# Kernel optimization log

Measured on AMD Instinct MI355X. Metric: run time of the kernel, lower is better.

The kernel has to match this reference:

```python
import jax, jax.numpy as jnp
import numpy as np

N, C, DFF, TMAX = 4, 768, 3072, 20
RMS_EPS = 1e-6
SINK_EPS = 1e-6
POST_MULT = 2.0


def setup_inputs() -> dict:
    key = jax.random.key(0)
    ks = jax.random.split(key, 5)
    B, S = 4, 4096
    x = jax.random.normal(ks[0], (B, S, N, C), dtype=jnp.float32)
    phi = jax.random.normal(ks[1], (N * C, N * N + 2 * N), dtype=jnp.float32) * 0.02
    b = jnp.zeros((N * N + 2 * N,), dtype=jnp.float32)
    alpha_pre = jnp.ones((1,), dtype=jnp.float32)
    alpha_post = jnp.ones((1,), dtype=jnp.float32)
    alpha_res = jnp.ones((1,), dtype=jnp.float32)
    W1 = jax.random.normal(ks[2], (C, DFF), dtype=jnp.float32) * (1.0 / np.sqrt(C))
    b1 = jnp.zeros((DFF,), dtype=jnp.float32)
    W2 = jax.random.normal(ks[3], (DFF, C), dtype=jnp.float32) * (1.0 / np.sqrt(DFF))
    b2 = jnp.zeros((C,), dtype=jnp.float32)
    return {"x": x, "phi": phi, "b": b, "alpha_pre": alpha_pre,
            "alpha_post": alpha_post, "alpha_res": alpha_res,
            "W1": W1, "b1": b1, "W2": W2, "b2": b2}


def _sinkhorn(logits):
    # logits: (..., 16) -> doubly-stochastic (..., 4, 4); rows = logits[..., 4i:4i+4]
    r = logits.reshape(*logits.shape[:-1], N, N)
    r = jnp.exp(r - jnp.max(r, axis=-1, keepdims=True))
    for _ in range(TMAX):
        r = r / (jnp.sum(r, axis=-1, keepdims=True) + SINK_EPS)  # row normalize
        r = r / (jnp.sum(r, axis=-2, keepdims=True) + SINK_EPS)  # column normalize
    return r


def _mhc_forward(x, phi, b, alpha_pre, alpha_post, alpha_res, W1, b1, W2, b2):
    lead = x.shape[:-2]
    x_mat = x.reshape(-1, N * C)
    # fused RMS-norm + linear routing projection
    invr = jax.lax.rsqrt(jnp.mean(x_mat * x_mat, axis=-1, keepdims=True) + RMS_EPS)
    mix = (x_mat @ phi) * invr  # (T, n^2 + 2n)
    h_pre = jax.nn.sigmoid(mix[:, :N] * alpha_pre + b[:N]).reshape(*lead, N)
    h_post = (jax.nn.sigmoid(mix[:, N:2 * N] * alpha_post + b[N:2 * N]) * POST_MULT).reshape(*lead, N)
    h_res = _sinkhorn(mix[:, 2 * N:] * alpha_res + b[2 * N:]).reshape(*lead, N, N)
    # pre-aggregate n streams -> single full-width stream
    x_in = jnp.einsum('...nc,...n->...c', x, h_pre)
    # wrapped sublayer: baseline MLP at full width
    f_out = jax.nn.gelu(x_in @ W1 + b1, approximate=False) @ W2 + b2
    # residual stream mixing + post scatter
    res_gather = jnp.einsum('...ij,...jc->...ic', h_res, x)
    return res_gather + h_post[..., None] * f_out[..., None, :]


def reference(x, phi, b, alpha_pre, alpha_post, alpha_res, W1, b1, W2, b2):
    return _mhc_forward(x, phi, b, alpha_pre, alpha_post, alpha_res, W1, b1, W2, b2)
```

## Files before the change

### kernel.cpp

```cpp
#include <hip/hip_runtime.h>
#include <hip/hip_bf16.h>
#include <stdint.h>

#define NT   16384
#define C_   768
#define DFF_ 3072
#define KX   3072
#define NMIX 24
#define TB   64
#define KSPLIT 4
#define KSEG (KX / KSPLIT)

typedef __attribute__((ext_vector_type(8))) short shortx8;
typedef __attribute__((ext_vector_type(4))) float floatx4;

__device__ __forceinline__ short f2bf(float f) {
  union { float f; uint32_t u; } v; v.f = f;
  uint32_t r = v.u + 0x7fffu + ((v.u >> 16) & 1u);
  return (short)(r >> 16);
}

__device__ __forceinline__ float bf2f(short s) {
  union { uint32_t u; float f; } v;
  v.u = ((uint32_t)(uint16_t)s) << 16;
  return v.f;
}

__device__ __forceinline__ float gelu_f(float v) {
  float u = 1.5957691216057308f * v * (1.0f + 0.044715f * v * v);
  return v / (1.0f + __expf(-u));
}

__global__ void phiT_kernel(const float* __restrict__ phi, float* __restrict__ phiT) {
  int idx = blockIdx.x * 256 + threadIdx.x;
  if (idx < KX * NMIX) {
    int k = idx / NMIX, j = idx - k * NMIX;
    phiT[(size_t)j * KX + k] = phi[idx];
  }
}

__global__ __launch_bounds__(256) void transpose_bf16(const float* __restrict__ in,
                                                      short* __restrict__ out,
                                                      int R, int C) {
  __shared__ float tile[32][33];
  int bx = blockIdx.x * 32;
  int by = blockIdx.y * 32;
  int tx = threadIdx.x & 31, ty = threadIdx.x >> 5;
  #pragma unroll
  for (int i = 0; i < 32; i += 8)
    tile[ty + i][tx] = in[(size_t)(by + ty + i) * C + bx + tx];
  __syncthreads();
  #pragma unroll
  for (int i = 0; i < 32; i += 8)
    out[(size_t)(bx + ty + i) * R + by + tx] = f2bf(tile[tx][ty + i]);
}

__global__ __launch_bounds__(256) void k1a(
    const float* __restrict__ x, const float* __restrict__ phiT,
    float* __restrict__ pmix, float* __restrict__ pssq) {
  __shared__ float xs[TB][132];
  int tid = threadIdx.x;
  int lane = tid & 63;
  int w = tid >> 6;
  int wu = __builtin_amdgcn_readfirstlane(w);
  int t0 = (blockIdx.x >> 2) * TB;
  int slot = blockIdx.x & 3;
  int ks = slot * KSEG;

  float acc[6] = {0.f, 0.f, 0.f, 0.f, 0.f, 0.f};
  float ssq = 0.f;

  for (int kc = ks; kc < ks + KSEG; kc += 128) {
    if (kc != ks) __syncthreads();
    #pragma unroll
    for (int jj = 0; jj < 8; ++jj) {
      int idx = tid + jj * 256;
      int row = idx >> 5, c4 = idx & 31;
      const float4 v = *(const float4*)&x[(size_t)(t0 + row) * KX + kc + c4 * 4];
      *(float4*)&xs[row][c4 * 4] = v;
    }
    __syncthreads();
    #pragma unroll 4
    for (int k4 = 0; k4 < 32; ++k4) {
      const float4 xv = *(const float4*)&xs[lane][k4 * 4];
      if (w == 0) ssq += xv.x * xv.x + xv.y * xv.y + xv.z * xv.z + xv.w * xv.w;
      int kk = kc + k4 * 4;
      #pragma unroll
      for (int jj = 0; jj < 6; ++jj) {
        const float4 p = *(const float4*)&phiT[(size_t)(wu * 6 + jj) * KX + kk];
        acc[jj] += p.x * xv.x + p.y * xv.y + p.z * xv.z + p.w * xv.w;
      }
    }
  }
  if (w == 0) pssq[(size_t)(t0 + lane) * KSPLIT + slot] = ssq;
  #pragma unroll
  for (int jj = 0; jj < 6; ++jj)
    pmix[((size_t)(t0 + lane) * KSPLIT + slot) * NMIX + wu * 6 + jj] = acc[jj];
}

__global__ __launch_bounds__(256) void k1b(
    const float* __restrict__ pmix, const float* __restrict__ pssq,
    const float* __restrict__ bvec, const float* __restrict__ a_pre,
    const float* __restrict__ a_post, const float* __restrict__ a_res,
    float* __restrict__ hpre, float* __restrict__ hpost, float* __restrict__ hres) {
  __shared__ float mixs[TB][NMIX];
  __shared__ float invr_s[TB];
  int tid = threadIdx.x;
  int t0 = blockIdx.x * TB;
  int tq = tid >> 2, r = tid & 3;

  {
    const float* pm = pmix + (size_t)(t0 + tq) * KSPLIT * NMIX;
    float s[6] = {0.f, 0.f, 0.f, 0.f, 0.f, 0.f};
    #pragma unroll
    for (int sl = 0; sl < KSPLIT; ++sl)
      #pragma unroll
      for (int jj = 0; jj < 6; ++jj)
        s[jj] += pm[sl * NMIX + r * 6 + jj];
    #pragma unroll
    for (int jj = 0; jj < 6; ++jj) mixs[tq][r * 6 + jj] = s[jj];
    if (r == 0) {
      const float* ps = pssq + (size_t)(t0 + tq) * KSPLIT;
      float sq = ps[0] + ps[1] + ps[2] + ps[3];
      invr_s[tq] = rsqrtf(sq * (1.0f / KX) + 1e-6f);
    }
  }
  __syncthreads();

  {
    float invr = invr_s[tq];
    float ares = a_res[0];
    float v0 = mixs[tq][8 + r * 4 + 0] * invr * ares + bvec[8 + r * 4 + 0];
    float v1 = mixs[tq][8 + r * 4 + 1] * invr * ares + bvec[8 + r * 4 + 1];
    float v2 = mixs[tq][8 + r * 4 + 2] * invr * ares + bvec[8 + r * 4 + 2];
    float v3 = mixs[tq][8 + r * 4 + 3] * invr * ares + bvec[8 + r * 4 + 3];
    float mx = fmaxf(fmaxf(v0, v1), fmaxf(v2, v3));
    v0 = __expf(v0 - mx); v1 = __expf(v1 - mx); v2 = __expf(v2 - mx); v3 = __expf(v3 - mx);
    for (int it = 0; it < 20; ++it) {
      float s = v0 + v1 + v2 + v3 + 1e-6f;
      float inv = 1.0f / s;
      v0 *= inv; v1 *= inv; v2 *= inv; v3 *= inv;
      float c0 = v0 + __shfl_xor(v0, 1); c0 += __shfl_xor(c0, 2);
      float c1 = v1 + __shfl_xor(v1, 1); c1 += __shfl_xor(c1, 2);
      float c2 = v2 + __shfl_xor(v2, 1); c2 += __shfl_xor(c2, 2);
      float c3 = v3 + __shfl_xor(v3, 1); c3 += __shfl_xor(c3, 2);
      v0 /= (c0 + 1e-6f); v1 /= (c1 + 1e-6f); v2 /= (c2 + 1e-6f); v3 /= (c3 + 1e-6f);
    }
    float* ho = hres + (size_t)(t0 + tq) * 16 + r * 4;
    ho[0] = v0; ho[1] = v1; ho[2] = v2; ho[3] = v3;
    if (r == 0) {
      float apre = a_pre[0];
      float4 hp;
      hp.x = 1.0f / (1.0f + __expf(-(mixs[tq][0] * invr * apre + bvec[0])));
      hp.y = 1.0f / (1.0f + __expf(-(mixs[tq][1] * invr * apre + bvec[1])));
      hp.z = 1.0f / (1.0f + __expf(-(mixs[tq][2] * invr * apre + bvec[2])));
      hp.w = 1.0f / (1.0f + __expf(-(mixs[tq][3] * invr * apre + bvec[3])));
      *(float4*)&hpre[(size_t)(t0 + tq) * 4] = hp;
    } else if (r == 1) {
      float apost = a_post[0];
      float4 hq;
      hq.x = 2.0f / (1.0f + __expf(-(mixs[tq][4] * invr * apost + bvec[4])));
      hq.y = 2.0f / (1.0f + __expf(-(mixs[tq][5] * invr * apost + bvec[5])));
      hq.z = 2.0f / (1.0f + __expf(-(mixs[tq][6] * invr * apost + bvec[6])));
      hq.w = 2.0f / (1.0f + __expf(-(mixs[tq][7] * invr * apost + bvec[7])));
      *(float4*)&hpost[(size_t)(t0 + tq) * 4] = hq;
    }
  }
}

__global__ __launch_bounds__(256) void k1c(
    const float* __restrict__ x, const float* __restrict__ hpre,
    short* __restrict__ x_in) {
  int idx = blockIdx.x * 256 + threadIdx.x;
  int t = idx / 192;
  int c = (idx - t * 192) * 4;
  float4 hp = *(const float4*)&hpre[(size_t)t * 4];
  const float* xr = x + (size_t)t * KX + c;
  float4 x0 = *(const float4*)(xr);
  float4 x1 = *(const float4*)(xr + C_);
  float4 x2 = *(const float4*)(xr + 2 * C_);
  float4 x3 = *(const float4*)(xr + 3 * C_);
  short4 s;
  s.x = f2bf(hp.x * x0.x + hp.y * x1.x + hp.z * x2.x + hp.w * x3.x);
  s.y = f2bf(hp.x * x0.y + hp.y * x1.y + hp.z * x2.y + hp.w * x3.y);
  s.z = f2bf(hp.x * x0.z + hp.y * x1.z + hp.z * x2.z + hp.w * x3.z);
  s.w = f2bf(hp.x * x0.w + hp.y * x1.w + hp.z * x2.w + hp.w * x3.w);
  *(short4*)&x_in[(size_t)t * C_ + c] = s;
}

template <int EPI>
__global__ __launch_bounds__(256, 3) void gemm_bt(
    const short* __restrict__ A, const short* __restrict__ B,
    int M, int N, int K, const float* __restrict__ bias,
    short* __restrict__ outb,
    const float* __restrict__ x, const float* __restrict__ hres,
    const float* __restrict__ hpost, float* __restrict__ out) {
  __shared__ __align__(16) char smem[34816];
  short* As = (short*)smem;
  short* Bs = (short*)(smem + 16384);
  short* cb = (short*)smem;
  int tid = threadIdx.x;
  int lane = tid & 63, w = tid >> 6;
  int nwg = gridDim.x * gridDim.y;
  int lid = blockIdx.y * gridDim.x + blockIdx.x;
  int sid = (lid & 7) * (nwg >> 3) + (lid >> 3);
  int bx = sid % gridDim.x, by = sid / gridDim.x;
  int m0 = by * 128, n0 = bx * 128;
  int wm = (w >> 1) * 64, wn = (w & 1) * 64;
  int lrow = lane & 15, quad = lane >> 4;
  floatx4 acc[4][4] = {};

  int srow = tid >> 2, sslot = tid & 3;
  int srow2 = (tid + 256) >> 2, sslot2 = (tid + 256) & 3;

  auto stage = [&](int buf, int k0) {
    const short* ga = A + (size_t)(m0 + srow) * K + k0 + sslot * 8;
    const short* gb = B + (size_t)(n0 + srow) * K + k0 + sslot * 8;
    __builtin_amdgcn_global_load_lds((const __attribute__((address_space(1))) void*)ga,
        (__attribute__((address_space(3))) void*)&As[buf * 4096 + tid * 8], 16, 0, 0);
    __builtin_amdgcn_global_load_lds((const __attribute__((address_space(1))) void*)gb,
        (__attribute__((address_space(3))) void*)&Bs[buf * 4096 + tid * 8], 16, 0, 0);
    const short* ga2 = A + (size_t)(m0 + srow2) * K + k0 + sslot2 * 8;
    const short* gb2 = B + (size_t)(n0 + srow2) * K + k0 + sslot2 * 8;
    __builtin_amdgcn_global_load_lds((const __attribute__((address_space(1))) void*)ga2,
        (__attribute__((address_space(3))) void*)&As[buf * 4096 + (tid + 256) * 8], 16, 0, 0);
    __builtin_amdgcn_global_load_lds((const __attribute__((address_space(1))) void*)gb2,
        (__attribute__((address_space(3))) void*)&Bs[buf * 4096 + (tid + 256) * 8], 16, 0, 0);
  };

  int ntiles = K >> 5;
  stage(0, 0);
  __syncthreads();
  int cur = 0;
  for (int t = 0; t < ntiles; ++t) {
    if (t + 1 < ntiles) stage(cur ^ 1, (t + 1) << 5);
    shortx8 af[4], bfr[4];
    #pragma unroll
    for (int mi = 0; mi < 4; ++mi)
      af[mi] = *(const shortx8*)&As[cur * 4096 + (wm + mi * 16 + lrow) * 32 + quad * 8];
    #pragma unroll
    for (int ni = 0; ni < 4; ++ni)
      bfr[ni] = *(const shortx8*)&Bs[cur * 4096 + (wn + ni * 16 + lrow) * 32 + quad * 8];
    #pragma unroll
    for (int mi = 0; mi < 4; ++mi)
      #pragma unroll
      for (int ni = 0; ni < 4; ++ni)
        acc[mi][ni] = __builtin_amdgcn_mfma_f32_16x16x32_bf16(af[mi], bfr[ni], acc[mi][ni], 0, 0, 0);
    __syncthreads();
    cur ^= 1;
  }

  float bcol[4];
  #pragma unroll
  for (int ni = 0; ni < 4; ++ni) bcol[ni] = bias[n0 + wn + ni * 16 + lrow];

  #pragma unroll
  for (int mi = 0; mi < 4; ++mi) {
    #pragma unroll
    for (int r = 0; r < 4; ++r) {
      int rr = wm + mi * 16 + quad * 4 + r;
      #pragma unroll
      for (int ni = 0; ni < 4; ++ni) {
        int col = wn + ni * 16 + lrow;
        float v = acc[mi][ni][r] + bcol[ni];
        if (EPI == 1) v = gelu_f(v);
        cb[rr * 136 + col] = f2bf(v);
      }
    }
  }
  __syncthreads();

  int rbase = tid >> 4, ic = tid & 15;
  if (EPI == 1) {
    #pragma unroll
    for (int v = 0; v < 8; ++v) {
      int rr = v * 16 + rbase;
      shortx8 val = *(const shortx8*)&cb[rr * 136 + ic * 8];
      *(shortx8*)&outb[(size_t)(m0 + rr) * N + n0 + ic * 8] = val;
    }
  } else {
    #pragma unroll
    for (int v = 0; v < 8; ++v) {
      int rr = v * 16 + rbase;
      int tr = m0 + rr;
      shortx8 f8 = *(const shortx8*)&cb[rr * 136 + ic * 8];
      float fv[8];
      #pragma unroll
      for (int j = 0; j < 8; ++j) fv[j] = bf2f(f8[j]);
      const float* xr = x + (size_t)tr * KX + n0 + ic * 8;
      float4 xa[4], xb[4];
      #pragma unroll
      for (int n = 0; n < 4; ++n) {
        xa[n] = *(const float4*)(xr + n * 768);
        xb[n] = *(const float4*)(xr + n * 768 + 4);
      }
      const float4* hrp = (const float4*)(hres + (size_t)tr * 16);
      float4 hp4 = *(const float4*)&hpost[(size_t)tr * 4];
      float hpv[4] = {hp4.x, hp4.y, hp4.z, hp4.w};
      float* orow = out + (size_t)tr * KX + n0 + ic * 8;
      #pragma unroll
      for (int n = 0; n < 4; ++n) {
        float4 h = hrp[n];
        float4 oa, ob;
        oa.x = h.x * xa[0].x + h.y * xa[1].x + h.z * xa[2].x + h.w * xa[3].x + hpv[n] * fv[0];
        oa.y = h.x * xa[0].y + h.y * xa[1].y + h.z * xa[2].y + h.w * xa[3].y + hpv[n] * fv[1];
        oa.z = h.x * xa[0].z + h.y * xa[1].z + h.z * xa[2].z + h.w * xa[3].z + hpv[n] * fv[2];
        oa.w = h.x * xa[0].w + h.y * xa[1].w + h.z * xa[2].w + h.w * xa[3].w + hpv[n] * fv[3];
        ob.x = h.x * xb[0].x + h.y * xb[1].x + h.z * xb[2].x + h.w * xb[3].x + hpv[n] * fv[4];
        ob.y = h.x * xb[0].y + h.y * xb[1].y + h.z * xb[2].y + h.w * xb[3].y + hpv[n] * fv[5];
        ob.z = h.x * xb[0].z + h.y * xb[1].z + h.z * xb[2].z + h.w * xb[3].z + hpv[n] * fv[6];
        ob.w = h.x * xb[0].w + h.y * xb[1].w + h.z * xb[2].w + h.w * xb[3].w + hpv[n] * fv[7];
        *(float4*)(orow + n * 768) = oa;
        *(float4*)(orow + n * 768 + 4) = ob;
      }
    }
  }
}

extern "C" void kernel_launch(void* const* d_in, const int* in_sizes, int n_in,
                              void* d_out, int out_size, void* d_ws, size_t ws_size,
                              hipStream_t stream) {
  const float* x      = (const float*)d_in[0];
  const float* phi    = (const float*)d_in[1];
  const float* b      = (const float*)d_in[2];
  const float* a_pre  = (const float*)d_in[3];
  const float* a_post = (const float*)d_in[4];
  const float* a_res  = (const float*)d_in[5];
  const float* W1     = (const float*)d_in[6];
  const float* b1     = (const float*)d_in[7];
  const float* W2     = (const float*)d_in[8];
  const float* b2     = (const float*)d_in[9];
  float* out = (float*)d_out;

  char* ws = (char*)d_ws;
  size_t off = 0;
  auto carve = [&](size_t bytes) {
    char* p = ws + off;
    off += (bytes + 255) & ~(size_t)255;
    return p;
  };
  short* x_in  = (short*)carve((size_t)NT * C_ * 2);
  short* act   = (short*)carve((size_t)NT * DFF_ * 2);
  float* hpost = (float*)carve((size_t)NT * 4 * 4);
  float* hres  = (float*)carve((size_t)NT * 16 * 4);
  float* hpre  = (float*)carve((size_t)NT * 4 * 4);
  short* W1T   = (short*)carve((size_t)DFF_ * C_ * 2);
  short* W2T   = (short*)carve((size_t)C_ * DFF_ * 2);
  float* phiT  = (float*)carve((size_t)NMIX * KX * 4);
  float* pmix  = (float*)carve((size_t)NT * KSPLIT * NMIX * 4);
  float* pssq  = (float*)carve((size_t)NT * KSPLIT * 4);

  phiT_kernel<<<dim3((KX * NMIX + 255) / 256), 256, 0, stream>>>(phi, phiT);
  transpose_bf16<<<dim3(DFF_ / 32, C_ / 32), 256, 0, stream>>>(W1, W1T, C_, DFF_);
  transpose_bf16<<<dim3(C_ / 32, DFF_ / 32), 256, 0, stream>>>(W2, W2T, DFF_, C_);
  k1a<<<dim3((NT / TB) * KSPLIT), 256, 0, stream>>>(x, phiT, pmix, pssq);
  k1b<<<dim3(NT / TB), 256, 0, stream>>>(pmix, pssq, b, a_pre, a_post, a_res,
                                         hpre, hpost, hres);
  k1c<<<dim3(NT * 192 / 256), 256, 0, stream>>>(x, hpre, x_in);
  gemm_bt<1><<<dim3(DFF_ / 128, NT / 128), 256, 0, stream>>>(
      x_in, W1T, NT, DFF_, C_, b1, act, nullptr, nullptr, nullptr, nullptr);
  gemm_bt<2><<<dim3(C_ / 128, NT / 128), 256, 0, stream>>>(
      act, W2T, NT, C_, DFF_, b2, nullptr, x, hres, hpost, out);
}
```

Baseline: 678.9 us.

## Triple-buffer GEMM LDS tiles with prefetch distance two and explicit waitcnts

Moves the bf16 GEMM main loop from double to triple buffering in LDS, prefetching tile t+2 while computing tile t. Per-iteration __syncthreads is replaced by explicit vmcnt/lgkmcnt waits plus s_barrier, so outstanding global->LDS loads can overlap across iterations. LDS grows from 34816 to 49152 bytes per block, which may limit occupancy at 3 blocks/CU, and the hand-tuned waitcnt counts must match the number of loads issued per stage.

```diff
diff --git a/kernel.cpp b/kernel.cpp
--- a/kernel.cpp
+++ b/kernel.cpp
@@ -195,9 +195,9 @@
     short* __restrict__ outb,
     const float* __restrict__ x, const float* __restrict__ hres,
     const float* __restrict__ hpost, float* __restrict__ out) {
-  __shared__ __align__(16) char smem[34816];
+  __shared__ __align__(16) char smem[49152];
   short* As = (short*)smem;
-  short* Bs = (short*)(smem + 16384);
+  short* Bs = (short*)(smem + 24576);
   short* cb = (short*)smem;
   int tid = threadIdx.x;
   int lane = tid & 63, w = tid >> 6;
@@ -213,42 +213,58 @@
   int srow = tid >> 2, sslot = tid & 3;
   int srow2 = (tid + 256) >> 2, sslot2 = (tid + 256) & 3;
 
-  auto stage = [&](int buf, int k0) {
+  auto stage = [&](int buf, int t) {
+    int k0 = t << 5;
+    int bo = buf << 12;
     const short* ga = A + (size_t)(m0 + srow) * K + k0 + sslot * 8;
     const short* gb = B + (size_t)(n0 + srow) * K + k0 + sslot * 8;
     __builtin_amdgcn_global_load_lds((const __attribute__((address_space(1))) void*)ga,
-        (__attribute__((address_space(3))) void*)&As[buf * 4096 + tid * 8], 16, 0, 0);
+        (__attribute__((address_space(3))) void*)&As[bo + tid * 8], 16, 0, 0);
     __builtin_amdgcn_global_load_lds((const __attribute__((address_space(1))) void*)gb,
-        (__attribute__((address_space(3))) void*)&Bs[buf * 4096 + tid * 8], 16, 0, 0);
+        (__attribute__((address_space(3))) void*)&Bs[bo + tid * 8], 16, 0, 0);
     const short* ga2 = A + (size_t)(m0 + srow2) * K + k0 + sslot2 * 8;
     const short* gb2 = B + (size_t)(n0 + srow2) * K + k0 + sslot2 * 8;
     __builtin_amdgcn_global_load_lds((const __attribute__((address_space(1))) void*)ga2,
-        (__attribute__((address_space(3))) void*)&As[buf * 4096 + (tid + 256) * 8], 16, 0, 0);
+        (__attribute__((address_space(3))) void*)&As[bo + (tid + 256) * 8], 16, 0, 0);
     __builtin_amdgcn_global_load_lds((const __attribute__((address_space(1))) void*)gb2,
-        (__attribute__((address_space(3))) void*)&Bs[buf * 4096 + (tid + 256) * 8], 16, 0, 0);
+        (__attribute__((address_space(3))) void*)&Bs[bo + (tid + 256) * 8], 16, 0, 0);
   };
 
   int ntiles = K >> 5;
   stage(0, 0);
-  __syncthreads();
-  int cur = 0;
+  stage(1, 1);
+  asm volatile("s_waitcnt vmcnt(4)" ::: "memory");
+  __builtin_amdgcn_s_barrier();
+  int cur = 0, pf = 2;
   for (int t = 0; t < ntiles; ++t) {
-    if (t + 1 < ntiles) stage(cur ^ 1, (t + 1) << 5);
+    bool do_pf = (t + 2 < ntiles);
     shortx8 af[4], bfr[4];
-    #pragma unroll
-    for (int mi = 0; mi < 4; ++mi)
-      af[mi] = *(const shortx8*)&As[cur * 4096 + (wm + mi * 16 + lrow) * 32 + quad * 8];
-    #pragma unroll
-    for (int ni = 0; ni < 4; ++ni)
-      bfr[ni] = *(const shortx8*)&Bs[cur * 4096 + (wn + ni * 16 + lrow) * 32 + quad * 8];
+    {
+      int co = cur << 12;
+      #pragma unroll
+      for (int mi = 0; mi < 4; ++mi)
+        af[mi] = *(const shortx8*)&As[co + (wm + mi * 16 + lrow) * 32 + quad * 8];
+      #pragma unroll
+      for (int ni = 0; ni < 4; ++ni)
+        bfr[ni] = *(const shortx8*)&Bs[co + (wn + ni * 16 + lrow) * 32 + quad * 8];
+    }
+    if (do_pf) stage(pf, t + 2);
+    asm volatile("s_waitcnt lgkmcnt(0)" ::: "memory");
+    __builtin_amdgcn_sched_barrier(0);
     #pragma unroll
     for (int mi = 0; mi < 4; ++mi)
       #pragma unroll
       for (int ni = 0; ni < 4; ++ni)
         acc[mi][ni] = __builtin_amdgcn_mfma_f32_16x16x32_bf16(af[mi], bfr[ni], acc[mi][ni], 0, 0, 0);
-    __syncthreads();
-    cur ^= 1;
-  }
+    if (t + 1 < ntiles) {
+      if (do_pf) asm volatile("s_waitcnt vmcnt(4)" ::: "memory");
+      else       asm volatile("s_waitcnt vmcnt(0)" ::: "memory");
+      __builtin_amdgcn_s_barrier();
+    }
+    cur = (cur == 2) ? 0 : cur + 1;
+    pf  = (pf  == 2) ? 0 : pf  + 1;
+  }
+  __syncthreads();
 
   float bcol[4];
   #pragma unroll
```

New measurement: 678.4 us. No clear change (-0.1%).
